# Kernel tuning notes

Hardware: AMD Instinct MI355X
Metric: run time of the kernel (lower is better)

Reference implementation:

```python
import jax, jax.numpy as jnp
import numpy as np

HIDDEN = 2048
NUM_HEADS = 16
NUM_KV_HEADS = 4
HEAD_DIM = HIDDEN // NUM_HEADS  # 128
GROUPS = NUM_HEADS // NUM_KV_HEADS  # 4
ROPE_DIMS = 32
QK_GAIN = 6.0
B, T = 2, 2048


def _rope_cos_sin(T, dtype):
    pos = jnp.arange(T, dtype=jnp.float32)
    inv_freq = 1.0 / (10000.0 ** (jnp.arange(0, ROPE_DIMS, 2, dtype=jnp.float32) / ROPE_DIMS))
    freqs = jnp.outer(pos, inv_freq)                  # [T, ROPE/2]
    freqs = jnp.concatenate([freqs, freqs], axis=-1)  # [T, ROPE]
    return jnp.cos(freqs).astype(dtype), jnp.sin(freqs).astype(dtype)


def _apply_rope(t, cos_f, sin_f):
    # t: [B, H, T, head_dim]; rope on first ROPE_DIMS, pass-through on the rest
    t_rt, t_pass = t[..., :ROPE_DIMS], t[..., ROPE_DIMS:]
    h1, h2 = jnp.split(t_rt, 2, axis=-1)
    rot = jnp.concatenate([-h2, h1], axis=-1)
    return jnp.concatenate([t_rt * cos_f + rot * sin_f, t_pass], axis=-1)


def setup_inputs() -> dict:
    key = jax.random.key(0)
    ks = jax.random.split(key, 5)
    s = 0.02
    return {
        "x": jax.random.normal(ks[0], (B, T, HIDDEN), jnp.float32),
        "Wq": jax.random.normal(ks[1], (HIDDEN, HIDDEN), jnp.float32) * s,
        "Wk": jax.random.normal(ks[2], (HIDDEN, NUM_KV_HEADS * HEAD_DIM), jnp.float32) * s,
        "Wv": jax.random.normal(ks[3], (HIDDEN, NUM_KV_HEADS * HEAD_DIM), jnp.float32) * s,
        "Wo": jax.random.normal(ks[4], (HIDDEN, HIDDEN), jnp.float32) * s,
    }


def reference(x, Wq, Wk, Wv, Wo):
    Bx, Tx, C = x.shape
    q = (x @ Wq).reshape(Bx, Tx, NUM_HEADS, HEAD_DIM).transpose(0, 2, 1, 3)      # [B,H,T,d]
    k = (x @ Wk).reshape(Bx, Tx, NUM_KV_HEADS, HEAD_DIM).transpose(0, 2, 1, 3)   # [B,KV,T,d]
    v = (x @ Wv).reshape(Bx, Tx, NUM_KV_HEADS, HEAD_DIM).transpose(0, 2, 1, 3)   # [B,KV,T,d]

    cos_f, sin_f = _rope_cos_sin(Tx, q.dtype)  # [T, ROPE]
    q = _apply_rope(q, cos_f, sin_f)
    k = _apply_rope(k, cos_f, sin_f)

    # GQA: group query heads per kv head instead of repeat_interleave-ing K/V
    qg = q.reshape(Bx, NUM_KV_HEADS, GROUPS, Tx, HEAD_DIM)
    scale = QK_GAIN / jnp.sqrt(jnp.asarray(HEAD_DIM, q.dtype))
    scores = jnp.einsum('bkgqd,bkld->bkgql', qg * scale, k)  # [B,KV,G,T,T]
    causal = jnp.tril(jnp.ones((Tx, Tx), dtype=bool))
    scores = jnp.where(causal, scores, jnp.asarray(-jnp.inf, scores.dtype))
    probs = jax.nn.softmax(scores, axis=-1)
    out = jnp.einsum('bkgql,bkld->bkgqd', probs, v)          # [B,KV,G,T,d]
    out = out.reshape(Bx, NUM_HEADS, Tx, HEAD_DIM).transpose(0, 2, 1, 3).reshape(Bx, Tx, C)
    return out @ Wo
```

## Files before the change

### kernel.cpp

```cpp
#include <hip/hip_runtime.h>
#include <hip/hip_bf16.h>
#include <cstdint>
#include <cstddef>

typedef unsigned short u16;
typedef short s16x8 __attribute__((ext_vector_type(8)));
typedef float f32x4 __attribute__((ext_vector_type(4)));
typedef float f32x16 __attribute__((ext_vector_type(16)));
typedef u16 u16x4 __attribute__((ext_vector_type(4)));

#define HIDDEN_C 2048
#define TSEQ 2048
#define BATCH 2
#define NHEADS 16
#define NKV 4
#define HDIM 128
#define NQKV 3072
#define BTR 4096
#define QK_SCALE 0.53033008588991f

__device__ __forceinline__ float bf2f(u16 u) {
  union { uint32_t i; float f; } v; v.i = ((uint32_t)u) << 16; return v.f;
}
__device__ __forceinline__ u16 f2bf(float f) {
  union { float f; uint32_t i; } v; v.f = f;
  uint32_t r = v.i + 0x7fffu + ((v.i >> 16) & 1u);
  return (u16)(r >> 16);
}

#define AS1(p) ((__attribute__((address_space(1))) void*)(uintptr_t)(p))
#define AS3(p) ((__attribute__((address_space(3))) void*)(p))

__global__ void convert_x_kernel(const float* __restrict__ x, u16* __restrict__ xb,
                                 float2* __restrict__ tab) {
  int gi = blockIdx.x * blockDim.x + threadIdx.x;
  if (gi < TSEQ * 16) {
    int t = gi >> 4, i = gi & 15;
    float f = powf(10000.f, -(float)i * (1.f / 16.f));
    float ang = (float)t * f;
    tab[gi] = make_float2(cosf(ang), sinf(ang));
  }
  int i = gi * 8;
  float4 a = *(const float4*)(x + i);
  float4 b = *(const float4*)(x + i + 4);
  uint4 o;
  o.x = (uint32_t)f2bf(a.x) | ((uint32_t)f2bf(a.y) << 16);
  o.y = (uint32_t)f2bf(a.z) | ((uint32_t)f2bf(a.w) << 16);
  o.z = (uint32_t)f2bf(b.x) | ((uint32_t)f2bf(b.y) << 16);
  o.w = (uint32_t)f2bf(b.z) | ((uint32_t)f2bf(b.w) << 16);
  *(uint4*)(xb + i) = o;
}

__global__ void transpose_w_kernel(const float* __restrict__ Wq,
                                   const float* __restrict__ Wk,
                                   const float* __restrict__ Wv,
                                   const float* __restrict__ Wo,
                                   u16* __restrict__ wqkvT,
                                   u16* __restrict__ woT) {
  const int z = blockIdx.z;
  const float* in; u16* out; int C;
  switch (z) {
    case 0: in = Wq; out = wqkvT;                        C = 2048; break;
    case 1: in = Wk; out = wqkvT + (size_t)2048 * 2048;  C = 512;  break;
    case 2: in = Wv; out = wqkvT + (size_t)2560 * 2048;  C = 512;  break;
    default: in = Wo; out = woT;                         C = 2048; break;
  }
  int r0 = blockIdx.y * 32, c0 = blockIdx.x * 32;
  if (c0 >= C) return;
  __shared__ float tile[32][33];
  int tx = threadIdx.x, ty = threadIdx.y;
  #pragma unroll
  for (int i = 0; i < 32; i += 8)
    tile[ty + i][tx] = in[(size_t)(r0 + ty + i) * C + c0 + tx];
  __syncthreads();
  #pragma unroll
  for (int i = 0; i < 32; i += 8)
    out[(size_t)(c0 + ty + i) * 2048 + r0 + tx] = f2bf(tile[tx][ty + i]);
}

template <typename OutT>
__global__ __launch_bounds__(256) void gemm_bt_kernel(const u16* __restrict__ A,
                                                      const u16* __restrict__ BT,
                                                      OutT* __restrict__ C,
                                                      int M, int N, int K,
                                                      const float2* __restrict__ tab,
                                                      int mode) {
  __shared__ u16 As[128 * 64];
  __shared__ u16 Bs[128 * 64];
  const int tid = threadIdx.x;
  const int wave = tid >> 6, lane = tid & 63;
  const int lr = lane & 15, lg = lane >> 4;
  const int m0 = blockIdx.y * 128, n0 = blockIdx.x * 128;
  const int wr = wave >> 1, wc = wave & 1;
  const int fsw = (lr & 7) << 3;
  f32x4 acc[4][4];
  #pragma unroll
  for (int a = 0; a < 4; ++a)
    #pragma unroll
    for (int b = 0; b < 4; ++b) acc[a][b] = (f32x4){0.f, 0.f, 0.f, 0.f};

  for (int k0 = 0; k0 < K; k0 += 64) {
    #pragma unroll
    for (int i = 0; i < 4; ++i) {
      int c = tid + i * 256;
      int row = c >> 3, slot = c & 7;
      int gslot = slot ^ (row & 7);
      const u16* gA = A + (size_t)(m0 + row) * K + k0 + gslot * 8;
      const u16* gB = BT + (size_t)(n0 + row) * K + k0 + gslot * 8;
      char* lA = (char*)As + (size_t)c * 16;
      char* lB = (char*)Bs + (size_t)c * 16;
      __builtin_amdgcn_global_load_lds(AS1(gA), AS3(lA), 16, 0, 0);
      __builtin_amdgcn_global_load_lds(AS1(gB), AS3(lB), 16, 0, 0);
    }
    __syncthreads();
    #pragma unroll
    for (int kk = 0; kk < 2; ++kk) {
      s16x8 af[4], bfr[4];
      #pragma unroll
      for (int mi = 0; mi < 4; ++mi)
        af[mi] = *(const s16x8*)(As + (wr * 64 + mi * 16 + lr) * 64 + ((kk * 32 + lg * 8) ^ fsw));
      #pragma unroll
      for (int ni = 0; ni < 4; ++ni)
        bfr[ni] = *(const s16x8*)(Bs + (wc * 64 + ni * 16 + lr) * 64 + ((kk * 32 + lg * 8) ^ fsw));
      #pragma unroll
      for (int mi = 0; mi < 4; ++mi)
        #pragma unroll
        for (int ni = 0; ni < 4; ++ni)
          acc[mi][ni] = __builtin_amdgcn_mfma_f32_16x16x32_bf16(af[mi], bfr[ni], acc[mi][ni], 0, 0, 0);
    }
    __syncthreads();
  }
  if (mode) {
    if (n0 < 2560 && wc == 0) {
      #pragma unroll
      for (int mi = 0; mi < 4; ++mi) {
        int rowb = m0 + wr * 64 + mi * 16 + lg * 4;
        #pragma unroll
        for (int r = 0; r < 4; ++r) {
          int t = (rowb + r) & (TSEQ - 1);
          float2 cs = tab[(t << 4) | lr];
          float a = acc[mi][0][r], b2 = acc[mi][1][r];
          acc[mi][0][r] = a * cs.x - b2 * cs.y;
          acc[mi][1][r] = b2 * cs.x + a * cs.y;
        }
      }
    }
    if (n0 < 2048) {
      #pragma unroll
      for (int mi = 0; mi < 4; ++mi)
        #pragma unroll
        for (int ni = 0; ni < 4; ++ni)
          #pragma unroll
          for (int r = 0; r < 4; ++r) acc[mi][ni][r] *= QK_SCALE;
    }
  }
  #pragma unroll
  for (int mi = 0; mi < 4; ++mi) {
    int rowb = m0 + wr * 64 + mi * 16 + lg * 4;
    #pragma unroll
    for (int ni = 0; ni < 4; ++ni) {
      int col = n0 + wc * 64 + ni * 16 + lr;
      #pragma unroll
      for (int r = 0; r < 4; ++r) {
        float v = acc[mi][ni][r];
        if constexpr (sizeof(OutT) == 2) C[(size_t)(rowb + r) * N + col] = (OutT)f2bf(v);
        else                             C[(size_t)(rowb + r) * N + col] = v;
      }
    }
  }
}

__global__ void transpose_v_kernel(const u16* __restrict__ qkv, u16* __restrict__ vt) {
  int bg = blockIdx.z;
  int b = bg >> 2, g = bg & 3;
  int t0 = blockIdx.x * 32, d0 = blockIdx.y * 32;
  __shared__ u16 tile[32][33];
  int tx = threadIdx.x, ty = threadIdx.y;
  #pragma unroll
  for (int i = 0; i < 32; i += 8)
    tile[ty + i][tx] = qkv[(size_t)(b * TSEQ + t0 + ty + i) * NQKV + 2560 + g * HDIM + d0 + tx];
  __syncthreads();
  #pragma unroll
  for (int i = 0; i < 32; i += 8)
    vt[((size_t)bg * HDIM + d0 + ty + i) * TSEQ + t0 + tx] = tile[tx][ty + i];
}

__global__ __launch_bounds__(256, 2) void attn_kernel(const u16* __restrict__ qkv,
                                                      const u16* __restrict__ vt,
                                                      u16* __restrict__ attn_out) {
  __shared__ u16 K_lds[2][64][128];
  __shared__ u16 V_lds[2][128][64];
  __shared__ u16 P_lds[4][32][64];

  const int idx = blockIdx.x;
  const int h = idx & 15, b = (idx >> 4) & 1, g = h >> 2;
  const int jb = (idx >> 5) & 7;
  const int tile = (idx >> 8) ? jb : 15 - jb;
  const int tid = threadIdx.x, w = tid >> 6, lane = tid & 63;
  const int lq = lane & 31;
  const int hf = lane >> 5;
  const int q0 = tile * 128;
  const int q0w = q0 + w * 32;
  const int swz = (lane & 7) << 3;
  const int pswz = lq & 7;

  const u16* Qg = qkv + (size_t)b * TSEQ * NQKV + h * HDIM;
  const u16* Kg = qkv + (size_t)b * TSEQ * NQKV + HIDDEN_C + g * HDIM;
  const u16* Vg = vt + (size_t)(b * NKV + g) * HDIM * TSEQ;

  s16x8 aq[8];
  {
    const u16* qrow = Qg + (size_t)(q0w + lq) * NQKV + hf * 8;
    #pragma unroll
    for (int ds = 0; ds < 8; ++ds) aq[ds] = *(const s16x8*)(qrow + ds * 16);
  }

  f32x16 O[4];
  #pragma unroll
  for (int dt = 0; dt < 4; ++dt)
    #pragma unroll
    for (int r = 0; r < 16; ++r) O[dt][r] = 0.f;
  float m_r = -1e30f, l_r = 0.f;

  auto STAGE = [&](int buf, int kb) {
    #pragma unroll
    for (int i = 0; i < 4; ++i) {
      int c = tid + i * 256;
      int row = c >> 4, slot = c & 15;
      int gslot = slot ^ (row & 7);
      const u16* src = Kg + (size_t)(kb + row) * NQKV + gslot * 8;
      char* dst = (char*)&K_lds[buf][0][0] + (size_t)c * 16;
      __builtin_amdgcn_global_load_lds(AS1(src), AS3(dst), 16, 0, 0);
    }
    #pragma unroll
    for (int i = 0; i < 4; ++i) {
      int c = tid + i * 256;
      int row = c >> 3, slot = c & 7;
      int gslot = slot ^ (row & 7);
      const u16* src = Vg + (size_t)row * TSEQ + kb + gslot * 8;
      char* dst = (char*)&V_lds[buf][0][0] + (size_t)c * 16;
      __builtin_amdgcn_global_load_lds(AS1(src), AS3(dst), 16, 0, 0);
    }
  };

  const int nt = (q0 + 128) / 64;
  STAGE(0, 0);
  asm volatile("s_waitcnt vmcnt(0)" ::: "memory");
  __syncthreads();

  for (int t = 0; t < nt; ++t) {
    const int kb = t * 64;
    const int cur = t & 1;
    if (t + 1 < nt) STAGE(cur ^ 1, kb + 64);

    if (kb <= q0w + 31) {
      f32x16 S[2];
      #pragma unroll
      for (int kh = 0; kh < 2; ++kh)
        #pragma unroll
        for (int r = 0; r < 16; ++r) S[kh][r] = 0.f;
      __builtin_amdgcn_s_setprio(1);
      #pragma unroll
      for (int kh = 0; kh < 2; ++kh) {
        const u16* krow = &K_lds[cur][kh * 32 + lq][0];
        #pragma unroll
        for (int ds = 0; ds < 8; ++ds) {
          s16x8 ak = *(const s16x8*)(krow + ((ds * 16 + hf * 8) ^ swz));
          S[kh] = __builtin_amdgcn_mfma_f32_32x32x16_bf16(ak, aq[ds], S[kh], 0, 0, 0);
        }
      }
      __builtin_amdgcn_s_setprio(0);
      if (kb + 63 > q0w) {
        const int q = q0w + lq;
        #pragma unroll
        for (int kh = 0; kh < 2; ++kh)
          #pragma unroll
          for (int r = 0; r < 16; ++r) {
            int k = kb + kh * 32 + (r & 3) + 8 * (r >> 2) + 4 * hf;
            if (k > q) S[kh][r] = -1e30f;
          }
      }
      f32x16 pm;
      #pragma unroll
      for (int r = 0; r < 16; ++r) pm[r] = fmaxf(S[0][r], S[1][r]);
      float m8[8];
      #pragma unroll
      for (int r = 0; r < 8; ++r) m8[r] = fmaxf(pm[r], pm[r + 8]);
      float mx = fmaxf(fmaxf(fmaxf(m8[0], m8[4]), fmaxf(m8[1], m8[5])),
                       fmaxf(fmaxf(m8[2], m8[6]), fmaxf(m8[3], m8[7])));
      mx = fmaxf(mx, __shfl_xor(mx, 32));
      const float mn = fmaxf(m_r, mx);
      const float al = __expf(m_r - mn);
      m_r = mn;
      #pragma unroll
      for (int kh = 0; kh < 2; ++kh)
        #pragma unroll
        for (int r = 0; r < 16; ++r) S[kh][r] = __expf(S[kh][r] - mn);
      f32x16 sv;
      #pragma unroll
      for (int r = 0; r < 16; ++r) sv[r] = S[0][r] + S[1][r];
      float s8[8];
      #pragma unroll
      for (int r = 0; r < 8; ++r) s8[r] = sv[r] + sv[r + 8];
      float ps = ((s8[0] + s8[4]) + (s8[1] + s8[5])) + ((s8[2] + s8[6]) + (s8[3] + s8[7]));
      ps += __shfl_xor(ps, 32);
      l_r = l_r * al + ps;
      #pragma unroll
      for (int dt = 0; dt < 4; ++dt)
        #pragma unroll
        for (int r = 0; r < 16; ++r) O[dt][r] *= al;
      u16* pw = &P_lds[w][lq][0];
      #pragma unroll
      for (int kh = 0; kh < 2; ++kh)
        #pragma unroll
        for (int r2 = 0; r2 < 4; ++r2) {
          u16x4 hq;
          #pragma unroll
          for (int j = 0; j < 4; ++j) hq[j] = f2bf(S[kh][r2 * 4 + j]);
          int slot = kh * 4 + r2;
          *(u16x4*)(pw + ((slot ^ pswz) << 3) + hf * 4) = hq;
        }
      asm volatile("s_waitcnt lgkmcnt(0)" ::: "memory");
      __builtin_amdgcn_sched_barrier(0);
      s16x8 pb[4];
      #pragma unroll
      for (int ks = 0; ks < 4; ++ks) {
        int slot = ks * 2 + hf;
        pb[ks] = *(const s16x8*)(pw + ((slot ^ pswz) << 3));
      }
      __builtin_amdgcn_s_setprio(1);
      #pragma unroll
      for (int dt = 0; dt < 4; ++dt) {
        const u16* vrow = &V_lds[cur][dt * 32 + lq][0];
        #pragma unroll
        for (int ks = 0; ks < 4; ++ks) {
          s16x8 av = *(const s16x8*)(vrow + ((ks * 16 + hf * 8) ^ swz));
          O[dt] = __builtin_amdgcn_mfma_f32_32x32x16_bf16(av, pb[ks], O[dt], 0, 0, 0);
        }
      }
      __builtin_amdgcn_s_setprio(0);
    }
    asm volatile("s_waitcnt vmcnt(0)" ::: "memory");
    __syncthreads();
  }

  const float invl = 1.f / l_r;
  u16* orow = attn_out + (size_t)(b * TSEQ + q0w + lq) * HIDDEN_C + h * HDIM + hf * 4;
  #pragma unroll
  for (int dt = 0; dt < 4; ++dt)
    #pragma unroll
    for (int r2 = 0; r2 < 4; ++r2) {
      u16x4 o4;
      #pragma unroll
      for (int j = 0; j < 4; ++j) o4[j] = f2bf(O[dt][r2 * 4 + j] * invl);
      *(u16x4*)(orow + dt * 32 + r2 * 8) = o4;
    }
}

extern "C" void kernel_launch(void* const* d_in, const int* in_sizes, int n_in,
                              void* d_out, int out_size, void* d_ws, size_t ws_size,
                              hipStream_t stream) {
  const float* x  = (const float*)d_in[0];
  const float* Wq = (const float*)d_in[1];
  const float* Wk = (const float*)d_in[2];
  const float* Wv = (const float*)d_in[3];
  const float* Wo = (const float*)d_in[4];
  float* out = (float*)d_out;
  char* ws = (char*)d_ws;

  u16* xb    = (u16*)(ws);
  u16* wqkvT = (u16*)(ws + (size_t)(16u << 20));
  u16* woT   = (u16*)(ws + (size_t)(28u << 20));
  u16* qkv   = (u16*)(ws + (size_t)(36u << 20));
  u16* vtb   = (u16*)(ws + (size_t)(60u << 20));
  u16* attn  = (u16*)(ws + (size_t)(64u << 20));
  float2* rope_tab = (float2*)(ws + (size_t)(64u << 20));

  dim3 tb(32, 8);
  convert_x_kernel<<<(BTR * HIDDEN_C / 8) / 256, 256, 0, stream>>>(x, xb, rope_tab);
  transpose_w_kernel<<<dim3(64, 64, 4), tb, 0, stream>>>(Wq, Wk, Wv, Wo, wqkvT, woT);

  gemm_bt_kernel<u16><<<dim3(NQKV / 128, BTR / 128), 256, 0, stream>>>(
      xb, wqkvT, qkv, BTR, NQKV, HIDDEN_C, rope_tab, 1);

  transpose_v_kernel<<<dim3(TSEQ / 32, HDIM / 32, BATCH * NKV), tb, 0, stream>>>(qkv, vtb);

  attn_kernel<<<512, 256, 0, stream>>>(qkv, vtb, attn);

  gemm_bt_kernel<float><<<dim3(HIDDEN_C / 128, BTR / 128), 256, 0, stream>>>(
      attn, woT, out, BTR, HIDDEN_C, HIDDEN_C, nullptr, 0);
}
```

Measured before the change: 210.8 us.

## Fuse prep kernels, write V transposed from QKV GEMM, lazy softmax rescale

The x conversion and weight transposes now run as one prep launch. The QKV GEMM epilogue writes V directly in transposed layout, which removes the separate transpose kernel and its extra pass over V. In attention, the K LDS swizzle is widened to 16 slots to cut bank conflicts, and the running-max rescale of O and l is skipped unless the new max exceeds the old one by more than 8. That lazy rescale trades exact max tracking for bounded exponent growth, and the V stores from the GEMM are strided 8-byte writes.

```diff
diff --git a/kernel.cpp b/kernel.cpp
--- a/kernel.cpp
+++ b/kernel.cpp
@@ -31,33 +31,37 @@
 #define AS1(p) ((__attribute__((address_space(1))) void*)(uintptr_t)(p))
 #define AS3(p) ((__attribute__((address_space(3))) void*)(p))
 
-__global__ void convert_x_kernel(const float* __restrict__ x, u16* __restrict__ xb,
-                                 float2* __restrict__ tab) {
-  int gi = blockIdx.x * blockDim.x + threadIdx.x;
-  if (gi < TSEQ * 16) {
-    int t = gi >> 4, i = gi & 15;
-    float f = powf(10000.f, -(float)i * (1.f / 16.f));
-    float ang = (float)t * f;
-    tab[gi] = make_float2(cosf(ang), sinf(ang));
-  }
-  int i = gi * 8;
-  float4 a = *(const float4*)(x + i);
-  float4 b = *(const float4*)(x + i + 4);
-  uint4 o;
-  o.x = (uint32_t)f2bf(a.x) | ((uint32_t)f2bf(a.y) << 16);
-  o.y = (uint32_t)f2bf(a.z) | ((uint32_t)f2bf(a.w) << 16);
-  o.z = (uint32_t)f2bf(b.x) | ((uint32_t)f2bf(b.y) << 16);
-  o.w = (uint32_t)f2bf(b.z) | ((uint32_t)f2bf(b.w) << 16);
-  *(uint4*)(xb + i) = o;
-}
-
-__global__ void transpose_w_kernel(const float* __restrict__ Wq,
-                                   const float* __restrict__ Wk,
-                                   const float* __restrict__ Wv,
-                                   const float* __restrict__ Wo,
-                                   u16* __restrict__ wqkvT,
-                                   u16* __restrict__ woT) {
+__global__ void prep_kernel(const float* __restrict__ x, u16* __restrict__ xb,
+                            float2* __restrict__ tab,
+                            const float* __restrict__ Wq,
+                            const float* __restrict__ Wk,
+                            const float* __restrict__ Wv,
+                            const float* __restrict__ Wo,
+                            u16* __restrict__ wqkvT,
+                            u16* __restrict__ woT) {
   const int z = blockIdx.z;
+  int tx = threadIdx.x, ty = threadIdx.y;
+  if (z == 4) {
+    int tid = ty * 32 + tx;
+    int bid = blockIdx.y * 64 + blockIdx.x;
+    int gi = bid * 256 + tid;
+    if (gi < TSEQ * 16) {
+      int t = gi >> 4, i = gi & 15;
+      float f = powf(10000.f, -(float)i * (1.f / 16.f));
+      float ang = (float)t * f;
+      tab[gi] = make_float2(cosf(ang), sinf(ang));
+    }
+    int i = gi * 8;
+    float4 a = *(const float4*)(x + i);
+    float4 b = *(const float4*)(x + i + 4);
+    uint4 o;
+    o.x = (uint32_t)f2bf(a.x) | ((uint32_t)f2bf(a.y) << 16);
+    o.y = (uint32_t)f2bf(a.z) | ((uint32_t)f2bf(a.w) << 16);
+    o.z = (uint32_t)f2bf(b.x) | ((uint32_t)f2bf(b.y) << 16);
+    o.w = (uint32_t)f2bf(b.z) | ((uint32_t)f2bf(b.w) << 16);
+    *(uint4*)(xb + i) = o;
+    return;
+  }
   const float* in; u16* out; int C;
   switch (z) {
     case 0: in = Wq; out = wqkvT;                        C = 2048; break;
@@ -68,7 +72,6 @@
   int r0 = blockIdx.y * 32, c0 = blockIdx.x * 32;
   if (c0 >= C) return;
   __shared__ float tile[32][33];
-  int tx = threadIdx.x, ty = threadIdx.y;
   #pragma unroll
   for (int i = 0; i < 32; i += 8)
     tile[ty + i][tx] = in[(size_t)(r0 + ty + i) * C + c0 + tx];
@@ -84,6 +87,7 @@
                                                       OutT* __restrict__ C,
                                                       int M, int N, int K,
                                                       const float2* __restrict__ tab,
+                                                      u16* __restrict__ vtb,
                                                       int mode) {
   __shared__ u16 As[128 * 64];
   __shared__ u16 Bs[128 * 64];
@@ -130,8 +134,25 @@
     }
     __syncthreads();
   }
+  if (mode && n0 >= 2560) {
+    #pragma unroll
+    for (int mi = 0; mi < 4; ++mi) {
+      int rowb = m0 + wr * 64 + mi * 16 + lg * 4;
+      int bidx = rowb >> 11, t = rowb & (TSEQ - 1);
+      #pragma unroll
+      for (int ni = 0; ni < 4; ++ni) {
+        int col = (n0 - 2560) + wc * 64 + ni * 16 + lr;
+        int gg = col >> 7, d = col & 127;
+        u16x4 o4;
+        #pragma unroll
+        for (int r = 0; r < 4; ++r) o4[r] = f2bf(acc[mi][ni][r]);
+        *(u16x4*)(vtb + ((size_t)(bidx * NKV + gg) * HDIM + d) * TSEQ + t) = o4;
+      }
+    }
+    return;
+  }
   if (mode) {
-    if (n0 < 2560 && wc == 0) {
+    if (wc == 0) {
       #pragma unroll
       for (int mi = 0; mi < 4; ++mi) {
         int rowb = m0 + wr * 64 + mi * 16 + lg * 4;
@@ -168,21 +189,6 @@
       }
     }
   }
-}
-
-__global__ void transpose_v_kernel(const u16* __restrict__ qkv, u16* __restrict__ vt) {
-  int bg = blockIdx.z;
-  int b = bg >> 2, g = bg & 3;
-  int t0 = blockIdx.x * 32, d0 = blockIdx.y * 32;
-  __shared__ u16 tile[32][33];
-  int tx = threadIdx.x, ty = threadIdx.y;
-  #pragma unroll
-  for (int i = 0; i < 32; i += 8)
-    tile[ty + i][tx] = qkv[(size_t)(b * TSEQ + t0 + ty + i) * NQKV + 2560 + g * HDIM + d0 + tx];
-  __syncthreads();
-  #pragma unroll
-  for (int i = 0; i < 32; i += 8)
-    vt[((size_t)bg * HDIM + d0 + ty + i) * TSEQ + t0 + tx] = tile[tx][ty + i];
 }
 
 __global__ __launch_bounds__(256, 2) void attn_kernel(const u16* __restrict__ qkv,
@@ -201,7 +207,8 @@
   const int hf = lane >> 5;
   const int q0 = tile * 128;
   const int q0w = q0 + w * 32;
-  const int swz = (lane & 7) << 3;
+  const int kswz = (lq & 15) << 3;
+  const int vswz = (lane & 7) << 3;
   const int pswz = lq & 7;
 
   const u16* Qg = qkv + (size_t)b * TSEQ * NQKV + h * HDIM;
@@ -227,7 +234,7 @@
     for (int i = 0; i < 4; ++i) {
       int c = tid + i * 256;
       int row = c >> 4, slot = c & 15;
-      int gslot = slot ^ (row & 7);
+      int gslot = slot ^ (row & 15);
       const u16* src = Kg + (size_t)(kb + row) * NQKV + gslot * 8;
       char* dst = (char*)&K_lds[buf][0][0] + (size_t)c * 16;
       __builtin_amdgcn_global_load_lds(AS1(src), AS3(dst), 16, 0, 0);
@@ -265,7 +272,7 @@
         const u16* krow = &K_lds[cur][kh * 32 + lq][0];
         #pragma unroll
         for (int ds = 0; ds < 8; ++ds) {
-          s16x8 ak = *(const s16x8*)(krow + ((ds * 16 + hf * 8) ^ swz));
+          s16x8 ak = *(const s16x8*)(krow + ((ds * 16 + hf * 8) ^ kswz));
           S[kh] = __builtin_amdgcn_mfma_f32_32x32x16_bf16(ak, aq[ds], S[kh], 0, 0, 0);
         }
       }
@@ -289,13 +296,20 @@
       float mx = fmaxf(fmaxf(fmaxf(m8[0], m8[4]), fmaxf(m8[1], m8[5])),
                        fmaxf(fmaxf(m8[2], m8[6]), fmaxf(m8[3], m8[7])));
       mx = fmaxf(mx, __shfl_xor(mx, 32));
-      const float mn = fmaxf(m_r, mx);
-      const float al = __expf(m_r - mn);
-      m_r = mn;
+      if (!__all(mx <= m_r + 8.f)) {
+        const float mn = fmaxf(m_r, mx);
+        const float al = __expf(m_r - mn);
+        m_r = mn;
+        l_r *= al;
+        #pragma unroll
+        for (int dt = 0; dt < 4; ++dt)
+          #pragma unroll
+          for (int r = 0; r < 16; ++r) O[dt][r] *= al;
+      }
       #pragma unroll
       for (int kh = 0; kh < 2; ++kh)
         #pragma unroll
-        for (int r = 0; r < 16; ++r) S[kh][r] = __expf(S[kh][r] - mn);
+        for (int r = 0; r < 16; ++r) S[kh][r] = __expf(S[kh][r] - m_r);
       f32x16 sv;
       #pragma unroll
       for (int r = 0; r < 16; ++r) sv[r] = S[0][r] + S[1][r];
@@ -304,11 +318,7 @@
       for (int r = 0; r < 8; ++r) s8[r] = sv[r] + sv[r + 8];
       float ps = ((s8[0] + s8[4]) + (s8[1] + s8[5])) + ((s8[2] + s8[6]) + (s8[3] + s8[7]));
       ps += __shfl_xor(ps, 32);
-      l_r = l_r * al + ps;
-      #pragma unroll
-      for (int dt = 0; dt < 4; ++dt)
-        #pragma unroll
-        for (int r = 0; r < 16; ++r) O[dt][r] *= al;
+      l_r += ps;
       u16* pw = &P_lds[w][lq][0];
       #pragma unroll
       for (int kh = 0; kh < 2; ++kh)
@@ -334,7 +344,7 @@
         const u16* vrow = &V_lds[cur][dt * 32 + lq][0];
         #pragma unroll
         for (int ks = 0; ks < 4; ++ks) {
-          s16x8 av = *(const s16x8*)(vrow + ((ks * 16 + hf * 8) ^ swz));
+          s16x8 av = *(const s16x8*)(vrow + ((ks * 16 + hf * 8) ^ vswz));
           O[dt] = __builtin_amdgcn_mfma_f32_32x32x16_bf16(av, pb[ks], O[dt], 0, 0, 0);
         }
       }
@@ -377,16 +387,13 @@
   float2* rope_tab = (float2*)(ws + (size_t)(64u << 20));
 
   dim3 tb(32, 8);
-  convert_x_kernel<<<(BTR * HIDDEN_C / 8) / 256, 256, 0, stream>>>(x, xb, rope_tab);
-  transpose_w_kernel<<<dim3(64, 64, 4), tb, 0, stream>>>(Wq, Wk, Wv, Wo, wqkvT, woT);
+  prep_kernel<<<dim3(64, 64, 5), tb, 0, stream>>>(x, xb, rope_tab, Wq, Wk, Wv, Wo, wqkvT, woT);
 
   gemm_bt_kernel<u16><<<dim3(NQKV / 128, BTR / 128), 256, 0, stream>>>(
-      xb, wqkvT, qkv, BTR, NQKV, HIDDEN_C, rope_tab, 1);
-
-  transpose_v_kernel<<<dim3(TSEQ / 32, HDIM / 32, BATCH * NKV), tb, 0, stream>>>(qkv, vtb);
+      xb, wqkvT, qkv, BTR, NQKV, HIDDEN_C, rope_tab, vtb, 1);
 
   attn_kernel<<<512, 256, 0, stream>>>(qkv, vtb, attn);
 
   gemm_bt_kernel<float><<<dim3(HIDDEN_C / 128, BTR / 128), 256, 0, stream>>>(
-      attn, woT, out, BTR, HIDDEN_C, HIDDEN_C, nullptr, 0);
-}
+      attn, woT, out, BTR, HIDDEN_C, HIDDEN_C, nullptr, nullptr, 0);
+}
```

Result: slower. 221.3 us (+5.0%).
